# Optimization experiments

Measured on AMD Instinct MI355X. Metric: run time of the kernel, lower is better.

The kernel has to match this reference:

```python
import jax, jax.numpy as jnp
import numpy as np
from jax import lax

NUM_LAYERS = 3
NUM_QUBITS = 8
BATCH = 131072
DIM = 2 ** NUM_QUBITS  # 256


def _rot_mats(params):
    # params: (L, Q, 3) angles for RX, RY, RZ. Returns combined U = RZ @ RY @ RX, (L, Q, 2, 2) complex64.
    half = params * 0.5
    cx = jnp.cos(half[..., 0]).astype(jnp.complex64)
    sx = jnp.sin(half[..., 0]).astype(jnp.complex64)
    cy = jnp.cos(half[..., 1]).astype(jnp.complex64)
    sy = jnp.sin(half[..., 1]).astype(jnp.complex64)
    ezm = jnp.exp(-1j * half[..., 2]).astype(jnp.complex64)
    ezp = jnp.exp(1j * half[..., 2]).astype(jnp.complex64)
    zero = jnp.zeros_like(cx)
    RX = jnp.stack([jnp.stack([cx, -1j * sx], -1), jnp.stack([-1j * sx, cx], -1)], -2)
    RY = jnp.stack([jnp.stack([cy, -sy], -1), jnp.stack([sy, cy], -1)], -2)
    RZ = jnp.stack([jnp.stack([ezm, zero], -1), jnp.stack([zero, ezp], -1)], -2)
    return jnp.einsum('lqij,lqjk,lqkm->lqim', RZ, RY, RX)


def _apply_1q(state, U, wire):
    # state: (B, 2,2,...,2); wire w lives on axis w+1 (PennyLane wire 0 = most significant bit)
    ax = wire + 1
    return jnp.moveaxis(jnp.tensordot(U, state, axes=((1,), (ax,))), 0, ax)


def _apply_cnot(state, ctrl, tgt):
    c_ax, t_ax = ctrl + 1, tgt + 1
    s0 = lax.index_in_dim(state, 0, axis=c_ax, keepdims=True)
    s1 = lax.index_in_dim(state, 1, axis=c_ax, keepdims=True)
    s1 = jnp.flip(s1, axis=t_ax)
    return jnp.concatenate([s0, s1], axis=c_ax)


def _circuit(params, state_re, state_im):
    U = _rot_mats(params)  # (L, Q, 2, 2)
    state = (state_re + 1j * state_im).astype(jnp.complex64)
    state = state.reshape((state.shape[0],) + (2,) * NUM_QUBITS)
    for l in range(NUM_LAYERS):
        for q in range(NUM_QUBITS):
            state = _apply_1q(state, U[l, q], q)
        for q in range(NUM_QUBITS):
            state = _apply_cnot(state, q, (q + 1) % NUM_QUBITS)
    state = state.reshape(state.shape[0], DIM)
    # probability that wire 0 measures |0>: sum |amp|^2 over first half of amplitudes
    half = state[:, : DIM // 2]
    return jnp.sum(half.real ** 2 + half.imag ** 2, axis=1).astype(jnp.float32)


def setup_inputs() -> dict:
    key = jax.random.key(0)
    k1, k2, k3 = jax.random.split(key, 3)
    params = jax.random.uniform(k1, (NUM_LAYERS, NUM_QUBITS, 3), dtype=jnp.float32)
    sr = jax.random.normal(k2, (BATCH, DIM), dtype=jnp.float32)
    si = jax.random.normal(k3, (BATCH, DIM), dtype=jnp.float32)
    norm = jnp.sqrt(jnp.sum(sr ** 2 + si ** 2, axis=1, keepdims=True))
    return {"params": params, "state_re": sr / norm, "state_im": si / norm}


def reference(params, state_re, state_im):
    return _circuit(params, state_re, state_im)
```

## Files before the change

kernel.cpp:

```cpp
#include <hip/hip_runtime.h>
#include <stdint.h>

#define NLAYERS 3
#define NQ 8
#define DIM 256
#define KDIM 512
#define BM 64
#define LDSTR 72

typedef float  f32x4  __attribute__((ext_vector_type(4)));
typedef __bf16 bf16x8 __attribute__((ext_vector_type(8)));

__device__ __forceinline__ unsigned short f2bf(float f){
    union { float f; uint32_t u; } v; v.f = f;
    uint32_t u = v.u;
    u += 0x7fffu + ((u >> 16) & 1u);
    return (unsigned short)(u >> 16);
}

__device__ __forceinline__ float2 cmul(float2 a, float2 b){
    return make_float2(a.x*b.x - a.y*b.y, a.x*b.y + a.y*b.x);
}

__global__ __launch_bounds__(256) void build_g_kernel(const float* __restrict__ params,
                                                      unsigned short* __restrict__ G){
    __shared__ float2 st[2][DIM];
    const int j = blockIdx.x;
    const int i = threadIdx.x;
    int cur = 0;
    st[0][i] = make_float2(i == j ? 1.0f : 0.0f, 0.0f);
    __syncthreads();

    for (int l = 0; l < NLAYERS; ++l){
        for (int q = 0; q < NQ; ++q){
            const float* pp = params + (l*NQ + q)*3;
            float hx = 0.5f*pp[0], hy = 0.5f*pp[1], hz = 0.5f*pp[2];
            float cx = cosf(hx), sx = sinf(hx);
            float cy = cosf(hy), sy = sinf(hy);
            float cz = cosf(hz), sz = sinf(hz);
            float2 ezm = make_float2(cz, -sz), ezp = make_float2(cz, sz);
            float2 m00 = make_float2( cy*cx,  sy*sx);
            float2 m01 = make_float2(-sy*cx, -cy*sx);
            float2 m10 = make_float2( sy*cx, -cy*sx);
            float2 m11 = make_float2( cy*cx, -sy*sx);
            float2 U0a = cmul(ezm, m00), U0b = cmul(ezm, m01);
            float2 U1a = cmul(ezp, m10), U1b = cmul(ezp, m11);
            int p  = 7 - q;
            int bs = (i >> p) & 1;
            int i0 = i & ~(1 << p), i1 = i | (1 << p);
            float2 a0 = st[cur][i0], a1 = st[cur][i1];
            float2 ua = bs ? U1a : U0a;
            float2 ub = bs ? U1b : U0b;
            float2 r;
            r.x = ua.x*a0.x - ua.y*a0.y + ub.x*a1.x - ub.y*a1.y;
            r.y = ua.x*a0.y + ua.y*a0.x + ub.x*a1.y + ub.y*a1.x;
            st[cur ^ 1][i] = r;
            cur ^= 1;
            __syncthreads();
        }
        for (int q = 0; q < NQ; ++q){
            int c  = 7 - q;
            int tb = 7 - ((q + 1) & 7);
            int src = ((i >> c) & 1) ? (i ^ (1 << tb)) : i;
            float2 r = st[cur][src];
            st[cur ^ 1][i] = r;
            cur ^= 1;
            __syncthreads();
        }
    }

    const int m = i & 127;
    float2 a = st[cur][m];
    unsigned short lo, hi;
    if (i < 128){ lo = f2bf(a.x); hi = f2bf(-a.y); }
    else        { lo = f2bf(a.y); hi = f2bf( a.x); }
    G[(size_t)i*KDIM + j]        = lo;
    G[(size_t)i*KDIM + j + DIM]  = hi;
}

__global__ __launch_bounds__(256, 3) void qform_kernel(const float* __restrict__ sr,
                                                       const float* __restrict__ si,
                                                       const unsigned short* __restrict__ G,
                                                       float* __restrict__ out){
    __shared__ unsigned short As[BM  * LDSTR];
    __shared__ unsigned short Bs[DIM * LDSTR];
    __shared__ float red[4 * BM];

    const int tid  = threadIdx.x;
    const int lane = tid & 63;
    const int w    = tid >> 6;
    const int l15  = lane & 15;
    const int quad = lane >> 4;
    const size_t mbase = (size_t)blockIdx.x * BM;

    const int arow = tid >> 2;
    const int aseg = tid & 3;

    f32x4 acc[4][4];
    const f32x4 vzero = {0.0f, 0.0f, 0.0f, 0.0f};
    #pragma unroll
    for (int ii = 0; ii < 4; ++ii)
        #pragma unroll
        for (int jj = 0; jj < 4; ++jj)
            acc[ii][jj] = vzero;

    for (int kc = 0; kc < 8; ++kc){
        __syncthreads();
        {
            const float* ga = ((kc < 4) ? sr : si)
                            + (mbase + arow)*(size_t)DIM + ((kc & 3)*64 + aseg*16);
            float4 f0 = ((const float4*)ga)[0];
            float4 f1 = ((const float4*)ga)[1];
            float4 f2 = ((const float4*)ga)[2];
            float4 f3 = ((const float4*)ga)[3];
            uint32_t pk[8];
            pk[0] = f2bf(f0.x) | ((uint32_t)f2bf(f0.y) << 16);
            pk[1] = f2bf(f0.z) | ((uint32_t)f2bf(f0.w) << 16);
            pk[2] = f2bf(f1.x) | ((uint32_t)f2bf(f1.y) << 16);
            pk[3] = f2bf(f1.z) | ((uint32_t)f2bf(f1.w) << 16);
            pk[4] = f2bf(f2.x) | ((uint32_t)f2bf(f2.y) << 16);
            pk[5] = f2bf(f2.z) | ((uint32_t)f2bf(f2.w) << 16);
            pk[6] = f2bf(f3.x) | ((uint32_t)f2bf(f3.y) << 16);
            pk[7] = f2bf(f3.z) | ((uint32_t)f2bf(f3.w) << 16);
            uint4* da = (uint4*)&As[arow*LDSTR + aseg*16];
            da[0] = make_uint4(pk[0], pk[1], pk[2], pk[3]);
            da[1] = make_uint4(pk[4], pk[5], pk[6], pk[7]);
        }
        #pragma unroll
        for (int pblk = 0; pblk < 4; ++pblk){
            int row = pblk*64 + arow;
            const uint4* gb = (const uint4*)(G + (size_t)row*KDIM + kc*64 + aseg*16);
            uint4 b0 = gb[0], b1 = gb[1];
            uint4* db = (uint4*)&Bs[row*LDSTR + aseg*16];
            db[0] = b0; db[1] = b1;
        }
        __syncthreads();

        #pragma unroll
        for (int ks = 0; ks < 2; ++ks){
            const int ko = ks*32 + quad*8;
            bf16x8 a[4], b[4];
            #pragma unroll
            for (int ii = 0; ii < 4; ++ii)
                a[ii] = *(const bf16x8*)&As[(ii*16 + l15)*LDSTR + ko];
            #pragma unroll
            for (int jj = 0; jj < 4; ++jj)
                b[jj] = *(const bf16x8*)&Bs[(w*64 + jj*16 + l15)*LDSTR + ko];
            #pragma unroll
            for (int ii = 0; ii < 4; ++ii)
                #pragma unroll
                for (int jj = 0; jj < 4; ++jj)
                    acc[ii][jj] = __builtin_amdgcn_mfma_f32_16x16x32_bf16(
                        a[ii], b[jj], acc[ii][jj], 0, 0, 0);
        }
    }

    float s[4][4];
    #pragma unroll
    for (int ii = 0; ii < 4; ++ii)
        #pragma unroll
        for (int r = 0; r < 4; ++r){
            float t = 0.0f;
            #pragma unroll
            for (int jj = 0; jj < 4; ++jj){ float v = acc[ii][jj][r]; t += v*v; }
            s[ii][r] = t;
        }
    #pragma unroll
    for (int ii = 0; ii < 4; ++ii)
        #pragma unroll
        for (int r = 0; r < 4; ++r){
            float t = s[ii][r];
            t += __shfl_xor(t, 1);
            t += __shfl_xor(t, 2);
            t += __shfl_xor(t, 4);
            t += __shfl_xor(t, 8);
            s[ii][r] = t;
        }
    if (l15 == 0){
        #pragma unroll
        for (int ii = 0; ii < 4; ++ii)
            #pragma unroll
            for (int r = 0; r < 4; ++r)
                red[w*64 + ii*16 + quad*4 + r] = s[ii][r];
    }
    __syncthreads();
    if (tid < 64){
        float o = red[tid] + red[64 + tid] + red[128 + tid] + red[192 + tid];
        out[mbase + tid] = o;
    }
}

extern "C" void kernel_launch(void* const* d_in, const int* in_sizes, int n_in,
                              void* d_out, int out_size, void* d_ws, size_t ws_size,
                              hipStream_t stream){
    const float* params = (const float*)d_in[0];
    const float* sr     = (const float*)d_in[1];
    const float* si     = (const float*)d_in[2];
    unsigned short* G   = (unsigned short*)d_ws;
    float* out          = (float*)d_out;

    build_g_kernel<<<dim3(DIM), dim3(256), 0, stream>>>(params, G);
    qform_kernel<<<dim3(131072 / BM), dim3(256), 0, stream>>>(sr, si, G, out);
}
```

Before: 306.3 us.

## Load tiles directly to LDS with XOR swizzle and truncate to bf16 on read

The GEMM kernel now uses global_load_lds to copy fp32 state and bf16 G tiles straight into LDS, with an XOR swizzle in place of the padded layout, so staging no longer passes through registers. The fp32 A tile is converted to bf16 by byte-permute truncation at LDS read time instead of round-to-nearest before storing. The G builder also precomputes the gate matrices once per block and collapses the eight CNOT permutations per layer into one composed permutation. The exchange is twice the LDS footprint for A, extra conversion work in the inner loop, and truncation instead of rounding, which adds a little error.

```diff
diff --git a/kernel.cpp b/kernel.cpp
--- a/kernel.cpp
+++ b/kernel.cpp
@@ -6,7 +6,7 @@
 #define DIM 256
 #define KDIM 512
 #define BM 64
-#define LDSTR 72
+#define NBLK (131072 / BM)
 
 typedef float  f32x4  __attribute__((ext_vector_type(4)));
 typedef __bf16 bf16x8 __attribute__((ext_vector_type(8)));
@@ -22,29 +22,53 @@
     return make_float2(a.x*b.x - a.y*b.y, a.x*b.y + a.y*b.x);
 }
 
+__device__ __forceinline__ void gload_lds16(void* lds, const void* g){
+    __builtin_amdgcn_global_load_lds(
+        (const __attribute__((address_space(1))) unsigned int*)g,
+        (__attribute__((address_space(3))) unsigned int*)lds,
+        16, 0, 0);
+}
+
 __global__ __launch_bounds__(256) void build_g_kernel(const float* __restrict__ params,
                                                       unsigned short* __restrict__ G){
     __shared__ float2 st[2][DIM];
+    __shared__ float2 gm[NLAYERS*NQ][4];
     const int j = blockIdx.x;
     const int i = threadIdx.x;
+
+    if (i < NLAYERS*NQ){
+        const float* pp = params + i*3;
+        float hx = 0.5f*pp[0], hy = 0.5f*pp[1], hz = 0.5f*pp[2];
+        float cx = cosf(hx), sx = sinf(hx);
+        float cy = cosf(hy), sy = sinf(hy);
+        float cz = cosf(hz), sz = sinf(hz);
+        float2 ezm = make_float2(cz, -sz), ezp = make_float2(cz, sz);
+        float2 m00 = make_float2( cy*cx,  sy*sx);
+        float2 m01 = make_float2(-sy*cx, -cy*sx);
+        float2 m10 = make_float2( sy*cx, -cy*sx);
+        float2 m11 = make_float2( cy*cx, -sy*sx);
+        gm[i][0] = cmul(ezm, m00);
+        gm[i][1] = cmul(ezm, m01);
+        gm[i][2] = cmul(ezp, m10);
+        gm[i][3] = cmul(ezp, m11);
+    }
+
+    int psrc = i;
+    #pragma unroll
+    for (int q = NQ-1; q >= 0; --q){
+        int c  = 7 - q;
+        int tb = 7 - ((q + 1) & 7);
+        psrc = ((psrc >> c) & 1) ? (psrc ^ (1 << tb)) : psrc;
+    }
+
     int cur = 0;
     st[0][i] = make_float2(i == j ? 1.0f : 0.0f, 0.0f);
     __syncthreads();
 
     for (int l = 0; l < NLAYERS; ++l){
         for (int q = 0; q < NQ; ++q){
-            const float* pp = params + (l*NQ + q)*3;
-            float hx = 0.5f*pp[0], hy = 0.5f*pp[1], hz = 0.5f*pp[2];
-            float cx = cosf(hx), sx = sinf(hx);
-            float cy = cosf(hy), sy = sinf(hy);
-            float cz = cosf(hz), sz = sinf(hz);
-            float2 ezm = make_float2(cz, -sz), ezp = make_float2(cz, sz);
-            float2 m00 = make_float2( cy*cx,  sy*sx);
-            float2 m01 = make_float2(-sy*cx, -cy*sx);
-            float2 m10 = make_float2( sy*cx, -cy*sx);
-            float2 m11 = make_float2( cy*cx, -sy*sx);
-            float2 U0a = cmul(ezm, m00), U0b = cmul(ezm, m01);
-            float2 U1a = cmul(ezp, m10), U1b = cmul(ezp, m11);
+            float2 U0a = gm[l*NQ+q][0], U0b = gm[l*NQ+q][1];
+            float2 U1a = gm[l*NQ+q][2], U1b = gm[l*NQ+q][3];
             int p  = 7 - q;
             int bs = (i >> p) & 1;
             int i0 = i & ~(1 << p), i1 = i | (1 << p);
@@ -58,15 +82,10 @@
             cur ^= 1;
             __syncthreads();
         }
-        for (int q = 0; q < NQ; ++q){
-            int c  = 7 - q;
-            int tb = 7 - ((q + 1) & 7);
-            int src = ((i >> c) & 1) ? (i ^ (1 << tb)) : i;
-            float2 r = st[cur][src];
-            st[cur ^ 1][i] = r;
-            cur ^= 1;
-            __syncthreads();
-        }
+        float2 r = st[cur][psrc];
+        st[cur ^ 1][i] = r;
+        cur ^= 1;
+        __syncthreads();
     }
 
     const int m = i & 127;
@@ -82,8 +101,8 @@
                                                        const float* __restrict__ si,
                                                        const unsigned short* __restrict__ G,
                                                        float* __restrict__ out){
-    __shared__ unsigned short As[BM  * LDSTR];
-    __shared__ unsigned short Bs[DIM * LDSTR];
+    __shared__ float          As[BM * 64];
+    __shared__ unsigned short Bs[DIM * 64];
     __shared__ float red[4 * BM];
 
     const int tid  = threadIdx.x;
@@ -91,10 +110,8 @@
     const int w    = tid >> 6;
     const int l15  = lane & 15;
     const int quad = lane >> 4;
+    const int x7   = l15 & 7;
     const size_t mbase = (size_t)blockIdx.x * BM;
-
-    const int arow = tid >> 2;
-    const int aseg = tid & 3;
 
     f32x4 acc[4][4];
     const f32x4 vzero = {0.0f, 0.0f, 0.0f, 0.0f};
@@ -107,45 +124,52 @@
     for (int kc = 0; kc < 8; ++kc){
         __syncthreads();
         {
-            const float* ga = ((kc < 4) ? sr : si)
-                            + (mbase + arow)*(size_t)DIM + ((kc & 3)*64 + aseg*16);
-            float4 f0 = ((const float4*)ga)[0];
-            float4 f1 = ((const float4*)ga)[1];
-            float4 f2 = ((const float4*)ga)[2];
-            float4 f3 = ((const float4*)ga)[3];
-            uint32_t pk[8];
-            pk[0] = f2bf(f0.x) | ((uint32_t)f2bf(f0.y) << 16);
-            pk[1] = f2bf(f0.z) | ((uint32_t)f2bf(f0.w) << 16);
-            pk[2] = f2bf(f1.x) | ((uint32_t)f2bf(f1.y) << 16);
-            pk[3] = f2bf(f1.z) | ((uint32_t)f2bf(f1.w) << 16);
-            pk[4] = f2bf(f2.x) | ((uint32_t)f2bf(f2.y) << 16);
-            pk[5] = f2bf(f2.z) | ((uint32_t)f2bf(f2.w) << 16);
-            pk[6] = f2bf(f3.x) | ((uint32_t)f2bf(f3.y) << 16);
-            pk[7] = f2bf(f3.z) | ((uint32_t)f2bf(f3.w) << 16);
-            uint4* da = (uint4*)&As[arow*LDSTR + aseg*16];
-            da[0] = make_uint4(pk[0], pk[1], pk[2], pk[3]);
-            da[1] = make_uint4(pk[4], pk[5], pk[6], pk[7]);
-        }
-        #pragma unroll
-        for (int pblk = 0; pblk < 4; ++pblk){
-            int row = pblk*64 + arow;
-            const uint4* gb = (const uint4*)(G + (size_t)row*KDIM + kc*64 + aseg*16);
-            uint4 b0 = gb[0], b1 = gb[1];
-            uint4* db = (uint4*)&Bs[row*LDSTR + aseg*16];
-            db[0] = b0; db[1] = b1;
+            const float* Zsrc = (kc < 4) ? sr : si;
+            const int kcol = (kc & 3) * 64;
+            #pragma unroll
+            for (int i = 0; i < 4; ++i){
+                const int c  = w*4 + i;
+                const int ar = c*4 + (lane >> 4);
+                const int gg = (lane & 15) ^ (ar & 7);
+                const float* gp = Zsrc + (mbase + ar)*DIM + kcol + gg*4;
+                gload_lds16(&As[c*256], gp);
+            }
+        }
+        {
+            #pragma unroll
+            for (int i = 0; i < 8; ++i){
+                const int c  = w*8 + i;
+                const int rb = c*8 + (lane >> 3);
+                const int gb = (lane & 7) ^ (rb & 7);
+                const unsigned short* gp = G + (size_t)rb*KDIM + kc*64 + gb*8;
+                gload_lds16(&Bs[c*512], gp);
+            }
         }
         __syncthreads();
 
         #pragma unroll
         for (int ks = 0; ks < 2; ++ks){
-            const int ko = ks*32 + quad*8;
             bf16x8 a[4], b[4];
-            #pragma unroll
-            for (int ii = 0; ii < 4; ++ii)
-                a[ii] = *(const bf16x8*)&As[(ii*16 + l15)*LDSTR + ko];
-            #pragma unroll
-            for (int jj = 0; jj < 4; ++jj)
-                b[jj] = *(const bf16x8*)&Bs[(w*64 + jj*16 + l15)*LDSTR + ko];
+            const int g0 = ks*8 + quad*2;
+            #pragma unroll
+            for (int ii = 0; ii < 4; ++ii){
+                const int m = ii*16 + l15;
+                union { float4 v; uint32_t u[4]; } h0, h1;
+                h0.v = *(const float4*)&As[m*64 + ((g0    ) ^ x7)*4];
+                h1.v = *(const float4*)&As[m*64 + ((g0 + 1) ^ x7)*4];
+                union { uint32_t u[4]; bf16x8 f; } pk;
+                pk.u[0] = __builtin_amdgcn_perm(h0.u[1], h0.u[0], 0x07060302);
+                pk.u[1] = __builtin_amdgcn_perm(h0.u[3], h0.u[2], 0x07060302);
+                pk.u[2] = __builtin_amdgcn_perm(h1.u[1], h1.u[0], 0x07060302);
+                pk.u[3] = __builtin_amdgcn_perm(h1.u[3], h1.u[2], 0x07060302);
+                a[ii] = pk.f;
+            }
+            const int gB = ks*4 + quad;
+            #pragma unroll
+            for (int jj = 0; jj < 4; ++jj){
+                const int n = w*64 + jj*16 + l15;
+                b[jj] = *(const bf16x8*)&Bs[n*64 + (gB ^ x7)*8];
+            }
             #pragma unroll
             for (int ii = 0; ii < 4; ++ii)
                 #pragma unroll
@@ -200,5 +224,5 @@
     float* out          = (float*)d_out;
 
     build_g_kernel<<<dim3(DIM), dim3(256), 0, stream>>>(params, G);
-    qform_kernel<<<dim3(131072 / BM), dim3(256), 0, stream>>>(sr, si, G, out);
-}
+    qform_kernel<<<dim3(NBLK), dim3(256), 0, stream>>>(sr, si, G, out);
+}
```

New measurement: 289.3 us. 5.5% less time.
